# Optimization experiments

Measured on AMD Instinct MI355X. Metric: run time of the kernel, lower is better.

## Reference

```python
import jax, jax.numpy as jnp
import numpy as np

DIM = 1024
N_HEADS = 16
HEAD_DIM = DIM // N_HEADS
MLP_RATIO = 4
LN_EPS = 1e-5


def _layer_norm(x, w):
    xf = x.astype(jnp.float32)
    mu = jnp.mean(xf, axis=-1, keepdims=True)
    var = jnp.var(xf, axis=-1, keepdims=True)
    y = (xf - mu) / jnp.sqrt(var + LN_EPS)
    return y * w[None, None, :]


def _apply_rope(x, cos, sin):
    # x: (b, s, h, d); cos, sin: (s, d/2)
    c = jnp.concatenate([cos, cos], axis=-1)[None, :, None, :]  # (1,s,1,d)
    s_ = jnp.concatenate([sin, sin], axis=-1)[None, :, None, :]
    x1, x2 = jnp.split(x, 2, axis=-1)
    rot = jnp.concatenate([-x2, x1], axis=-1)
    return x * c + rot * s_


def setup_inputs() -> dict:
    key = jax.random.key(0)
    ks = jax.random.split(key, 12)
    b, s = 2, 2048
    x = jax.random.normal(ks[0], (b, s, DIM), dtype=jnp.float32)
    rot_cos = jax.random.uniform(ks[1], (1, s, 1, 1, HEAD_DIM), dtype=jnp.float32)
    rot_sin = jax.random.uniform(ks[2], (1, s, 1, 1, HEAD_DIM), dtype=jnp.float32)
    w_init = 0.02
    params = {
        'ln1_w': jnp.ones((DIM,), jnp.float32),
        'w_qkv': jax.random.normal(ks[3], (3 * DIM, DIM), jnp.float32) * w_init,
        'w_out': jax.random.normal(ks[4], (DIM, DIM), jnp.float32) * w_init,
        'ln2_w': jnp.ones((DIM,), jnp.float32),
        'w_mlp1': jax.random.normal(ks[5], (MLP_RATIO * DIM, DIM), jnp.float32) * w_init,
        'b_mlp1': jnp.zeros((MLP_RATIO * DIM,), jnp.float32),
        'w_mlp2': jax.random.normal(ks[6], (DIM, MLP_RATIO * DIM), jnp.float32) * w_init,
        'b_mlp2': jnp.zeros((DIM,), jnp.float32),
    }
    return {'x': x, 'rot_cos': rot_cos, 'rot_sin': rot_sin, **params}


def reference(x, rot_cos, rot_sin, ln1_w, w_qkv, w_out, ln2_w, w_mlp1, b_mlp1, w_mlp2, b_mlp2):
    b, s, _ = x.shape
    # _split_rotary: (1,s,1,1,hd) -> (s, hd/2)
    cos = rot_cos[0, :, 0, 0, : HEAD_DIM // 2]
    sin = rot_sin[0, :, 0, 0, : HEAD_DIM // 2]

    x_skip = x
    h1 = _layer_norm(x, ln1_w)
    qkv = jnp.einsum('bsd,ed->bse', h1, w_qkv).reshape(b, s, 3, N_HEADS, HEAD_DIM)
    q, k, v = qkv[:, :, 0], qkv[:, :, 1], qkv[:, :, 2]
    q = _apply_rope(q, cos, sin)
    k = _apply_rope(k, cos, sin)

    # causal SDPA, scale = 1/sqrt(head_dim) (flex_attention default)
    scale = 1.0 / np.sqrt(HEAD_DIM)
    scores = jnp.einsum('bqhd,bkhd->bhqk', q, k) * scale
    causal = jnp.tril(jnp.ones((s, s), dtype=bool))
    scores = jnp.where(causal[None, None], scores, -jnp.inf)
    attn = jax.nn.softmax(scores, axis=-1)
    o = jnp.einsum('bhqk,bkhd->bqhd', attn, v).reshape(b, s, DIM)

    # attn out + residual (eval: dropout off, scale=1)
    x = x_skip + jnp.einsum('bsd,ed->bse', o, w_out)

    # MLP with tanh GELU + residual
    h2 = _layer_norm(x, ln2_w)
    u = jnp.einsum('bsd,ed->bse', h2, w_mlp1) + b_mlp1
    u = jax.nn.gelu(u, approximate=True)
    m = jnp.einsum('bse,de->bsd', u, w_mlp2) + b_mlp2
    return x + m
```

## Files before the change

kernel.cpp:

```cpp
#include <hip/hip_runtime.h>
#include <hip/hip_bf16.h>
#include <math.h>


#define B_ 2
#define S_ 2048
#define D_ 1024
#define H_ 16
#define DH_ 64
#define MLP_ 4096
#define ROWS_ (B_ * S_)

typedef short bf16x8 __attribute__((ext_vector_type(8)));
typedef float f32x4 __attribute__((ext_vector_type(4)));
typedef unsigned short ushort_t;
typedef ushort_t u16x4 __attribute__((ext_vector_type(4)));
typedef unsigned int u32x2 __attribute__((ext_vector_type(2)));

__device__ __forceinline__ float wave_reduce_sum(float v) {
  #pragma unroll
  for (int off = 32; off > 0; off >>= 1) v += __shfl_down(v, off, 64);
  return v;
}

__device__ __forceinline__ ushort_t f2bf(float v) {
  __hip_bfloat16 h = __float2bfloat16(v);
  return *(ushort_t*)&h;
}
__device__ __forceinline__ float bf2f(ushort_t u) {
  unsigned int v = ((unsigned int)u) << 16;
  union { unsigned int i; float f; } c; c.i = v; return c.f;
}

__device__ __forceinline__ float exp2_fast(float x) {
#if __has_builtin(__builtin_amdgcn_exp2f)
  return __builtin_amdgcn_exp2f(x);
#else
  return exp2f(x);
#endif
}
__device__ __forceinline__ float rcp_fast(float x) {
#if __has_builtin(__builtin_amdgcn_rcpf)
  return __builtin_amdgcn_rcpf(x);
#else
  return 1.0f / x;
#endif
}

__device__ __forceinline__ void async_copy16(const void* g, void* l) {
  __builtin_amdgcn_global_load_lds(
      (const __attribute__((address_space(1))) void*)g,
      (__attribute__((address_space(3))) void*)l, 16, 0, 0);
}

__global__ __launch_bounds__(256) void cast_w_kernel(
    const float* __restrict__ s0, ushort_t* __restrict__ d0, int n0,
    const float* __restrict__ s1, ushort_t* __restrict__ d1, int n1,
    const float* __restrict__ s2, ushort_t* __restrict__ d2, int n2,
    const float* __restrict__ s3, ushort_t* __restrict__ d3, int n3) {
  const float* s; ushort_t* d; int n;
  switch (blockIdx.y) {
    case 0: s = s0; d = d0; n = n0; break;
    case 1: s = s1; d = d1; n = n1; break;
    case 2: s = s2; d = d2; n = n2; break;
    default: s = s3; d = d3; n = n3; break;
  }
  const int i = (blockIdx.x * 256 + threadIdx.x) * 4;
  if (i < n) {
    const float4 v = *reinterpret_cast<const float4*>(s + i);
    u16x4 o;
    o[0] = f2bf(v.x); o[1] = f2bf(v.y); o[2] = f2bf(v.z); o[3] = f2bf(v.w);
    *reinterpret_cast<u16x4*>(d + i) = o;
  }
}

__global__ __launch_bounds__(256) void ln_kernel(
    const float* __restrict__ x, const float* __restrict__ w,
    ushort_t* __restrict__ y) {
  const int row = blockIdx.x;
  const float4 v = reinterpret_cast<const float4*>(x + (size_t)row * D_)[threadIdx.x];
  float s  = v.x + v.y + v.z + v.w;
  float ss = v.x * v.x + v.y * v.y + v.z * v.z + v.w * v.w;
  __shared__ float red[8];
  const int wave = threadIdx.x >> 6, lane = threadIdx.x & 63;
  const float ws1 = wave_reduce_sum(s);
  const float ws2 = wave_reduce_sum(ss);
  if (lane == 0) { red[wave] = ws1; red[4 + wave] = ws2; }
  __syncthreads();
  const float tot  = red[0] + red[1] + red[2] + red[3];
  const float tot2 = red[4] + red[5] + red[6] + red[7];
  const float mu  = tot * (1.0f / D_);
  const float var = tot2 * (1.0f / D_) - mu * mu;
  const float inv = rsqrtf(var + 1e-5f);
  const float4 wv = reinterpret_cast<const float4*>(w)[threadIdx.x];
  u16x4 o;
  o[0] = f2bf((v.x - mu) * inv * wv.x);
  o[1] = f2bf((v.y - mu) * inv * wv.y);
  o[2] = f2bf((v.z - mu) * inv * wv.z);
  o[3] = f2bf((v.w - mu) * inv * wv.w);
  reinterpret_cast<u16x4*>(y + (size_t)row * D_)[threadIdx.x] = o;
}

__device__ __forceinline__ float gelu_tanh(float u) {
  const float p = u + 0.044715f * u * u * u;
  const float e = exp2_fast(-2.3022078f * p);
  return u * rcp_fast(1.0f + e);
}

template <int FUSE, int OUTBF, int QKV>
__global__ __launch_bounds__(256) void gemm_bt(
    const ushort_t* __restrict__ A, const ushort_t* __restrict__ W,
    const float* __restrict__ bias, const float* __restrict__ res,
    void* __restrict__ Cv, ushort_t* __restrict__ VtOut,
    int M, int N, int K, int sm, int sn, int rects_n) {
  __shared__ ushort_t As[3][128 * 32];
  __shared__ ushort_t Bs[3][128 * 32];
  const int tid = threadIdx.x;
  const int wave = tid >> 6, lane = tid & 63;
  const int l15 = lane & 15, quad = lane >> 4;

  const int lin = blockIdx.x;
  const int xcd = lin & 7, j = lin >> 3;
  const int rm = xcd / rects_n, rn = xcd % rects_n;
  const int m0 = (rm * sm + (j % sm)) * 128;
  const int n0 = (rn * sn + (j / sm)) * 128;
  const int wm = (wave & 1) * 64, wn = (wave >> 1) * 64;

  const int srow = tid >> 2;
  const int gcol = (((tid & 3) ^ ((srow >> 1) & 3)) * 8);
  const ushort_t* Ag = A + (size_t)(m0 + srow) * K + gcol;
  const ushort_t* Wg = W + (size_t)(n0 + srow) * K + gcol;

  f32x4 acc[4][4] = {};
  const int rslot = (quad ^ ((l15 >> 1) & 3)) * 8;

  const int NI = K >> 5;
  async_copy16(Ag,               &As[0][tid * 8]);
  async_copy16(Ag + 64 * K,      &As[0][2048 + tid * 8]);
  async_copy16(Wg,               &Bs[0][tid * 8]);
  async_copy16(Wg + 64 * K,      &Bs[0][2048 + tid * 8]);
  if (NI > 1) {
    async_copy16(Ag + 32,          &As[1][tid * 8]);
    async_copy16(Ag + 64 * K + 32, &As[1][2048 + tid * 8]);
    async_copy16(Wg + 32,          &Bs[1][tid * 8]);
    async_copy16(Wg + 64 * K + 32, &Bs[1][2048 + tid * 8]);
  }

  int st = 0;
  for (int i = 0; i < NI; ++i) {
    if (i + 1 < NI) asm volatile("s_waitcnt vmcnt(4)" ::: "memory");
    else            asm volatile("s_waitcnt vmcnt(0)" ::: "memory");
    __builtin_amdgcn_s_barrier();
    __builtin_amdgcn_sched_barrier(0);
    if (i + 2 < NI) {
      const int k2 = (i + 2) << 5;
      const int nb = (st >= 1) ? st - 1 : st + 2;
      async_copy16(Ag + k2,          &As[nb][tid * 8]);
      async_copy16(Ag + 64 * K + k2, &As[nb][2048 + tid * 8]);
      async_copy16(Wg + k2,          &Bs[nb][tid * 8]);
      async_copy16(Wg + 64 * K + k2, &Bs[nb][2048 + tid * 8]);
    }
    bf16x8 af[4], bfr[4];
    #pragma unroll
    for (int ii = 0; ii < 4; ++ii) {
      af[ii]  = *(const bf16x8*)&As[st][(wm + ii * 16 + l15) * 32 + rslot];
      bfr[ii] = *(const bf16x8*)&Bs[st][(wn + ii * 16 + l15) * 32 + rslot];
    }
    #pragma unroll
    for (int ii = 0; ii < 4; ++ii)
      #pragma unroll
      for (int jj = 0; jj < 4; ++jj)
        acc[ii][jj] = __builtin_amdgcn_mfma_f32_16x16x32_bf16(af[ii], bfr[jj], acc[ii][jj], 0, 0, 0);
    st = (st == 2) ? 0 : st + 1;
  }

  #pragma unroll
  for (int i = 0; i < 4; ++i) {
    const int mb = m0 + wm + i * 16 + quad * 4;
    #pragma unroll
    for (int jj = 0; jj < 4; ++jj) {
      const int n = n0 + wn + jj * 16 + l15;
      float cv[4];
      #pragma unroll
      for (int r = 0; r < 4; ++r) {
        float c = acc[i][jj][r];
        if (FUSE & 1) c += bias[n];
        if (FUSE & 2) c = gelu_tanh(c);
        if (FUSE & 4) c += res[(size_t)(mb + r) * N + n];
        cv[r] = c;
      }
      if (QKV && ((n0 + wn) >> 10) == 2) {
        const int d  = n & 63;
        const int hh = (n >> 6) & 15;
        const int bb = mb >> 11;
        const int ss = mb & (S_ - 1);
        u16x4 pk;
        #pragma unroll
        for (int r = 0; r < 4; ++r) pk[r] = f2bf(cv[r]);
        *(u16x4*)&VtOut[((size_t)(bb * H_ + hh) * DH_ + d) * S_ + ss] = pk;
      } else {
        #pragma unroll
        for (int r = 0; r < 4; ++r) {
          if (OUTBF) ((ushort_t*)Cv)[(size_t)(mb + r) * N + n] = f2bf(cv[r]);
          else       ((float*)Cv)[(size_t)(mb + r) * N + n]   = cv[r];
        }
      }
    }
  }
}

template <int FUSE, int OUTBF>
__global__ __launch_bounds__(256) void gemm64_bt(
    const ushort_t* __restrict__ A, const ushort_t* __restrict__ W,
    const float* __restrict__ bias, const float* __restrict__ res,
    void* __restrict__ Cv, int M, int N, int K, int sm, int sn, int rects_n) {
  __shared__ ushort_t As[2][64 * 64];
  __shared__ ushort_t Bs[2][128 * 64];
  const int tid = threadIdx.x;
  const int wave = tid >> 6, lane = tid & 63;
  const int l15 = lane & 15, quad = lane >> 4;

  const int lin = blockIdx.x;
  const int xcd = lin & 7, j = lin >> 3;
  const int rm = xcd / rects_n, rn = xcd % rects_n;
  const int m0 = (rm * sm + (j % sm)) * 64;
  const int n0 = (rn * sn + (j / sm)) * 128;
  const int wn = wave * 32;

  const int srow = tid >> 3;
  const int gcol = (((tid & 7) ^ (srow & 7)) * 8);
  const ushort_t* Ag = A + (size_t)(m0 + srow) * K + gcol;
  const ushort_t* Wg = W + (size_t)(n0 + srow) * K + gcol;

  f32x4 acc[4][2] = {};

  const int NI = K >> 6;
  #pragma unroll
  for (int i = 0; i < 2; ++i)
    async_copy16(Ag + (size_t)i * 32 * K, &As[0][i * 2048 + tid * 8]);
  #pragma unroll
  for (int i = 0; i < 4; ++i)
    async_copy16(Wg + (size_t)i * 32 * K, &Bs[0][i * 2048 + tid * 8]);

  for (int it = 0; it < NI; ++it) {
    const int st = it & 1;
    __syncthreads();
    if (it + 1 < NI) {
      const int k1 = (it + 1) << 6;
      #pragma unroll
      for (int i = 0; i < 2; ++i)
        async_copy16(Ag + (size_t)i * 32 * K + k1, &As[1 - st][i * 2048 + tid * 8]);
      #pragma unroll
      for (int i = 0; i < 4; ++i)
        async_copy16(Wg + (size_t)i * 32 * K + k1, &Bs[1 - st][i * 2048 + tid * 8]);
    }
    #pragma unroll
    for (int kk = 0; kk < 2; ++kk) {
      const int slot = (((kk * 4 + quad) ^ (l15 & 7)) * 8);
      bf16x8 af[4], bfr[2];
      #pragma unroll
      for (int i = 0; i < 4; ++i)
        af[i] = *(const bf16x8*)&As[st][(i * 16 + l15) * 64 + slot];
      #pragma unroll
      for (int jj = 0; jj < 2; ++jj)
        bfr[jj] = *(const bf16x8*)&Bs[st][(wn + jj * 16 + l15) * 64 + slot];
      #pragma unroll
      for (int i = 0; i < 4; ++i)
        #pragma unroll
        for (int jj = 0; jj < 2; ++jj)
          acc[i][jj] = __builtin_amdgcn_mfma_f32_16x16x32_bf16(af[i], bfr[jj], acc[i][jj], 0, 0, 0);
    }
  }

  #pragma unroll
  for (int i = 0; i < 4; ++i) {
    const int mb = m0 + i * 16 + quad * 4;
    #pragma unroll
    for (int jj = 0; jj < 2; ++jj) {
      const int n = n0 + wn + jj * 16 + l15;
      #pragma unroll
      for (int r = 0; r < 4; ++r) {
        float c = acc[i][jj][r];
        if (FUSE & 1) c += bias[n];
        if (FUSE & 2) c = gelu_tanh(c);
        if (FUSE & 4) c += res[(size_t)(mb + r) * N + n];
        if (OUTBF) ((ushort_t*)Cv)[(size_t)(mb + r) * N + n] = f2bf(c);
        else       ((float*)Cv)[(size_t)(mb + r) * N + n]   = c;
      }
    }
  }
}

__global__ __launch_bounds__(256) void rope_kernel(
    const ushort_t* __restrict__ qkv, const float* __restrict__ cosb,
    const float* __restrict__ sinb, ushort_t* __restrict__ Qo,
    ushort_t* __restrict__ Ko) {
  const int bs = blockIdx.x;
  const int s  = bs & (S_ - 1);
  const int b  = bs >> 11;
  const int t  = threadIdx.x;
  const ushort_t* base = qkv + (size_t)bs * (3 * D_);
  #pragma unroll
  for (int i = 0; i < 8; ++i) {
    const int e = i * 256 + t;
    const int which = e >> 10;
    const int rem = e & 1023;
    const int h = rem >> 6;
    const int d = rem & 63;
    const float val = bf2f(base[e]);
    float out;
    if (d < 32) {
      out = val * cosb[s * 64 + d] - bf2f(base[e + 32]) * sinb[s * 64 + d];
    } else {
      out = val * cosb[s * 64 + d - 32] + bf2f(base[e - 32]) * sinb[s * 64 + d - 32];
    }
    const size_t oidx = (((size_t)(b * H_ + h)) * S_ + s) * DH_ + d;
    if (which == 0) Qo[oidx] = f2bf(out * 0.18033688736f);
    else            Ko[oidx] = f2bf(out);
  }
}

#define PPAD 72

__global__ __launch_bounds__(256) void attn_kernel(
    const ushort_t* __restrict__ Qb, const ushort_t* __restrict__ Kb,
    const ushort_t* __restrict__ Vt, ushort_t* __restrict__ O) {
  __shared__ ushort_t Ks[2][64 * 64];
  __shared__ ushort_t Vs[2][64 * 64];
  __shared__ ushort_t Plds[4][2][16 * PPAD];

  const int tid  = threadIdx.x;
  const int wave = tid >> 6;
  const int lane = tid & 63;
  const int l15 = lane & 15, quad = lane >> 4;

  const int lin = blockIdx.x;
  const int bh  = lin & 31;
  const int g   = 15 - (lin >> 5);
  const int b = bh >> 4, h = bh & 15;
  const int q0 = g * 128 + wave * 32;

  const int nch_w   = (q0 >> 6) + 1;
  const int nch_max = 2 * g + 2;

  const ushort_t* Kbh = Kb + (size_t)bh * S_ * DH_;
  const ushort_t* Vbh = Vt + (size_t)bh * DH_ * S_;

  auto stage = [&](int buf, int c) {
    const int k0s = c << 6;
    #pragma unroll
    for (int i = 0; i < 2; ++i) {
      const int idx  = i * 256 + tid;
      const int row  = idx >> 3;
      const int slot = idx & 7;
      const int scol = ((slot ^ (row & 7)) * 8);
      async_copy16(Kbh + (size_t)(k0s + row) * DH_ + scol, &Ks[buf][idx * 8]);
      async_copy16(Vbh + (size_t)row * S_ + k0s + scol,    &Vs[buf][idx * 8]);
    }
  };

  bf16x8 qb[2][2];
  #pragma unroll
  for (int t = 0; t < 2; ++t) {
    const ushort_t* qptr = Qb + ((size_t)bh * S_ + q0 + t * 16 + l15) * DH_ + quad * 8;
    qb[t][0] = *(const bf16x8*)(qptr);
    qb[t][1] = *(const bf16x8*)(qptr + 32);
  }

  f32x4 o_acc[2][4] = {};
  float m_run[2] = {-1e30f, -1e30f}, l_run[2] = {0.0f, 0.0f};

  stage(0, 0);

  for (int c = 0; c < nch_max; ++c) {
    const int st = c & 1;
    __syncthreads();
    if (c + 1 < nch_max) stage(st ^ 1, c + 1);
    if (c >= nch_w) continue;
    const int k0 = c << 6;

    bf16x8 ka[4][2];
    #pragma unroll
    for (int kt = 0; kt < 4; ++kt) {
      const int row = kt * 16 + l15;
      const int bse = row * 64, rx = row & 7;
      ka[kt][0] = *(const bf16x8*)&Ks[st][bse + ((quad ^ rx) * 8)];
      ka[kt][1] = *(const bf16x8*)&Ks[st][bse + (((4 + quad) ^ rx) * 8)];
    }

    f32x4 s_t[2][4];
    __builtin_amdgcn_s_setprio(1);
    #pragma unroll
    for (int t = 0; t < 2; ++t)
      #pragma unroll
      for (int kt = 0; kt < 4; ++kt) {
        f32x4 z = {0.0f, 0.0f, 0.0f, 0.0f};
        z = __builtin_amdgcn_mfma_f32_16x16x32_bf16(ka[kt][0], qb[t][0], z, 0, 0, 0);
        z = __builtin_amdgcn_mfma_f32_16x16x32_bf16(ka[kt][1], qb[t][1], z, 0, 0, 0);
        s_t[t][kt] = z;
      }
    __builtin_amdgcn_s_setprio(0);

    if (c == nch_w - 1) {
      #pragma unroll
      for (int t = 0; t < 2; ++t) {
        const int query = q0 + t * 16 + l15;
        #pragma unroll
        for (int kt = 0; kt < 4; ++kt)
          #pragma unroll
          for (int r = 0; r < 4; ++r)
            if (k0 + kt * 16 + quad * 4 + r > query) s_t[t][kt][r] = -1e30f;
      }
    }

    #pragma unroll
    for (int t = 0; t < 2; ++t) {
      float mx = -1e30f;
      #pragma unroll
      for (int kt = 0; kt < 4; ++kt)
        #pragma unroll
        for (int r = 0; r < 4; ++r) mx = fmaxf(mx, s_t[t][kt][r]);
      mx = fmaxf(mx, __shfl_xor(mx, 16, 64));
      mx = fmaxf(mx, __shfl_xor(mx, 32, 64));
      const float m_new = fmaxf(m_run[t], mx);
      const float alpha = exp2_fast(m_run[t] - m_new);
      float rs = 0.0f;
      #pragma unroll
      for (int kt = 0; kt < 4; ++kt)
        #pragma unroll
        for (int r = 0; r < 4; ++r) {
          const float e = exp2_fast(s_t[t][kt][r] - m_new);
          s_t[t][kt][r] = e;
          rs += e;
        }
      rs += __shfl_xor(rs, 16, 64);
      rs += __shfl_xor(rs, 32, 64);
      l_run[t] = l_run[t] * alpha + rs;
      m_run[t] = m_new;
      #pragma unroll
      for (int mt = 0; mt < 4; ++mt)
        #pragma unroll
        for (int r = 0; r < 4; ++r) o_acc[t][mt][r] *= alpha;
    }

    bf16x8 va[4][2];
    #pragma unroll
    for (int mt = 0; mt < 4; ++mt) {
      const int row = mt * 16 + l15;
      const int bse = row * 64, rx = row & 7;
      va[mt][0] = *(const bf16x8*)&Vs[st][bse + ((quad ^ rx) * 8)];
      va[mt][1] = *(const bf16x8*)&Vs[st][bse + (((4 + quad) ^ rx) * 8)];
    }

    #pragma unroll
    for (int t = 0; t < 2; ++t) {
      ushort_t* Pw = &Plds[wave][t][0];
      #pragma unroll
      for (int kt = 0; kt < 4; ++kt) {
        u32x2 wpair;
        wpair[0] = (unsigned)f2bf(s_t[t][kt][0]) | ((unsigned)f2bf(s_t[t][kt][1]) << 16);
        wpair[1] = (unsigned)f2bf(s_t[t][kt][2]) | ((unsigned)f2bf(s_t[t][kt][3]) << 16);
        *(u32x2*)&Pw[l15 * PPAD + kt * 16 + quad * 4] = wpair;
      }
      asm volatile("s_waitcnt lgkmcnt(0)" ::: "memory");
      const bf16x8 pb0 = *(const bf16x8*)&Pw[l15 * PPAD + quad * 8];
      const bf16x8 pb1 = *(const bf16x8*)&Pw[l15 * PPAD + 32 + quad * 8];
      __builtin_amdgcn_s_setprio(1);
      #pragma unroll
      for (int mt = 0; mt < 4; ++mt) {
        o_acc[t][mt] = __builtin_amdgcn_mfma_f32_16x16x32_bf16(va[mt][0], pb0, o_acc[t][mt], 0, 0, 0);
        o_acc[t][mt] = __builtin_amdgcn_mfma_f32_16x16x32_bf16(va[mt][1], pb1, o_acc[t][mt], 0, 0, 0);
      }
      __builtin_amdgcn_s_setprio(0);
    }
  }

  #pragma unroll
  for (int t = 0; t < 2; ++t) {
    const float inv = 1.0f / l_run[t];
    #pragma unroll
    for (int mt = 0; mt < 4; ++mt) {
      u16x4 pk;
      #pragma unroll
      for (int r = 0; r < 4; ++r) pk[r] = f2bf(o_acc[t][mt][r] * inv);
      *(u16x4*)&O[(((size_t)b * S_ + q0 + t * 16 + l15) * H_ + h) * DH_ + mt * 16 + quad * 4] = pk;
    }
  }
}

extern "C" void kernel_launch(void* const* d_in, const int* in_sizes, int n_in,
                              void* d_out, int out_size, void* d_ws, size_t ws_size,
                              hipStream_t stream) {
  const float* x       = (const float*)d_in[0];
  const float* rot_cos = (const float*)d_in[1];
  const float* rot_sin = (const float*)d_in[2];
  const float* ln1_w   = (const float*)d_in[3];
  const float* w_qkv   = (const float*)d_in[4];
  const float* w_out   = (const float*)d_in[5];
  const float* ln2_w   = (const float*)d_in[6];
  const float* w_mlp1  = (const float*)d_in[7];
  const float* b_mlp1  = (const float*)d_in[8];
  const float* w_mlp2  = (const float*)d_in[9];
  const float* b_mlp2  = (const float*)d_in[10];
  float* out = (float*)d_out;

  char* wsb = (char*)d_ws;
  const size_t MB = 1u << 20;
  ushort_t* h1_bf  = (ushort_t*)(wsb + 0 * MB);
  ushort_t* qkv_bf = (ushort_t*)(wsb + 8 * MB);
  ushort_t* q_bf   = (ushort_t*)(wsb + 32 * MB);
  ushort_t* k_bf   = (ushort_t*)(wsb + 40 * MB);
  ushort_t* v_t    = (ushort_t*)(wsb + 48 * MB);
  ushort_t* o_bf   = (ushort_t*)(wsb + 56 * MB);
  float*    x2     = (float*)   (wsb + 64 * MB);
  ushort_t* u_bf   = (ushort_t*)(wsb + 80 * MB);
  ushort_t* wq_bf  = (ushort_t*)(wsb + 112 * MB);
  ushort_t* wo_bf  = (ushort_t*)(wsb + 118 * MB);
  ushort_t* w1_bf  = (ushort_t*)(wsb + 120 * MB);
  ushort_t* w2_bf  = (ushort_t*)(wsb + 128 * MB);
  (void)ws_size; (void)in_sizes; (void)n_in; (void)out_size;

  dim3 b256(256);

  cast_w_kernel<<<dim3(4096, 4), b256, 0, stream>>>(
      w_qkv, wq_bf, 3 * D_ * D_, w_out, wo_bf, D_ * D_,
      w_mlp1, w1_bf, MLP_ * D_, w_mlp2, w2_bf, MLP_ * D_);
  ln_kernel<<<dim3(ROWS_), b256, 0, stream>>>(x, ln1_w, h1_bf);
  gemm_bt<0, 1, 1><<<dim3(768), b256, 0, stream>>>(
      h1_bf, wq_bf, nullptr, nullptr, qkv_bf, v_t, ROWS_, 3 * D_, D_, 16, 6, 4);
  rope_kernel<<<dim3(ROWS_), b256, 0, stream>>>(qkv_bf, rot_cos, rot_sin, q_bf, k_bf);
  attn_kernel<<<dim3(512), b256, 0, stream>>>(q_bf, k_bf, v_t, o_bf);
  gemm64_bt<4, 0><<<dim3(512), b256, 0, stream>>>(
      o_bf, wo_bf, nullptr, x, x2, ROWS_, D_, D_, 16, 4, 2);
  ln_kernel<<<dim3(ROWS_), b256, 0, stream>>>(x2, ln2_w, h1_bf);
  gemm_bt<3, 1, 0><<<dim3(1024), b256, 0, stream>>>(
      h1_bf, w1_bf, b_mlp1, nullptr, u_bf, nullptr, ROWS_, MLP_, D_, 16, 8, 4);
  gemm64_bt<5, 0><<<dim3(512), b256, 0, stream>>>(
      u_bf, w2_bf, b_mlp2, x2, out, ROWS_, D_, MLP_, 16, 4, 2);
}
```

Baseline: 364.4 us.

## Triple-buffer GEMM loads, reorder attention blocks, and skip lazy softmax rescales

The 64x128 GEMM moves from a double-buffered to a triple-buffered cp.async pipeline, prefetching two K-tiles ahead and replacing __syncthreads with a vmcnt wait plus s_barrier, so global-load latency is hidden better. The attention kernel changes its query-block launch order so the first half of blocks run heavy tiles in descending order and the rest ascending, to balance causal work. The online softmax skips the rescale of O and l whenever the new max exceeds the running max by at most 8 in log2 space, trading some exp headroom for less rescale work. Shared memory per GEMM block grows by half, which may lower occupancy.

After: 366.8 us. About the same (+0.7%).

```diff
diff --git a/kernel.cpp b/kernel.cpp
--- a/kernel.cpp
+++ b/kernel.cpp
@@ -214,8 +214,8 @@
     const ushort_t* __restrict__ A, const ushort_t* __restrict__ W,
     const float* __restrict__ bias, const float* __restrict__ res,
     void* __restrict__ Cv, int M, int N, int K, int sm, int sn, int rects_n) {
-  __shared__ ushort_t As[2][64 * 64];
-  __shared__ ushort_t Bs[2][128 * 64];
+  __shared__ ushort_t As[3][64 * 64];
+  __shared__ ushort_t Bs[3][128 * 64];
   const int tid = threadIdx.x;
   const int wave = tid >> 6, lane = tid & 63;
   const int l15 = lane & 15, quad = lane >> 4;
@@ -241,18 +241,30 @@
   #pragma unroll
   for (int i = 0; i < 4; ++i)
     async_copy16(Wg + (size_t)i * 32 * K, &Bs[0][i * 2048 + tid * 8]);
-
+  if (NI > 1) {
+    #pragma unroll
+    for (int i = 0; i < 2; ++i)
+      async_copy16(Ag + (size_t)i * 32 * K + 64, &As[1][i * 2048 + tid * 8]);
+    #pragma unroll
+    for (int i = 0; i < 4; ++i)
+      async_copy16(Wg + (size_t)i * 32 * K + 64, &Bs[1][i * 2048 + tid * 8]);
+  }
+
+  int st = 0;
   for (int it = 0; it < NI; ++it) {
-    const int st = it & 1;
-    __syncthreads();
-    if (it + 1 < NI) {
-      const int k1 = (it + 1) << 6;
+    if (it + 1 < NI) asm volatile("s_waitcnt vmcnt(6)" ::: "memory");
+    else             asm volatile("s_waitcnt vmcnt(0)" ::: "memory");
+    __builtin_amdgcn_s_barrier();
+    __builtin_amdgcn_sched_barrier(0);
+    if (it + 2 < NI) {
+      const int k2 = (it + 2) << 6;
+      const int nb = (st >= 1) ? st - 1 : st + 2;
       #pragma unroll
       for (int i = 0; i < 2; ++i)
-        async_copy16(Ag + (size_t)i * 32 * K + k1, &As[1 - st][i * 2048 + tid * 8]);
+        async_copy16(Ag + (size_t)i * 32 * K + k2, &As[nb][i * 2048 + tid * 8]);
       #pragma unroll
       for (int i = 0; i < 4; ++i)
-        async_copy16(Wg + (size_t)i * 32 * K + k1, &Bs[1 - st][i * 2048 + tid * 8]);
+        async_copy16(Wg + (size_t)i * 32 * K + k2, &Bs[nb][i * 2048 + tid * 8]);
     }
     #pragma unroll
     for (int kk = 0; kk < 2; ++kk) {
@@ -270,6 +282,7 @@
         for (int jj = 0; jj < 2; ++jj)
           acc[i][jj] = __builtin_amdgcn_mfma_f32_16x16x32_bf16(af[i], bfr[jj], acc[i][jj], 0, 0, 0);
     }
+    st = (st == 2) ? 0 : st + 1;
   }
 
   #pragma unroll
@@ -336,7 +349,8 @@
 
   const int lin = blockIdx.x;
   const int bh  = lin & 31;
-  const int g   = 15 - (lin >> 5);
+  const int u   = lin >> 5;
+  const int g   = (u < 8) ? (15 - u) : (u - 8);
   const int b = bh >> 4, h = bh & 15;
   const int q0 = g * 128 + wave * 32;
 
@@ -422,25 +436,28 @@
         for (int r = 0; r < 4; ++r) mx = fmaxf(mx, s_t[t][kt][r]);
       mx = fmaxf(mx, __shfl_xor(mx, 16, 64));
       mx = fmaxf(mx, __shfl_xor(mx, 32, 64));
-      const float m_new = fmaxf(m_run[t], mx);
-      const float alpha = exp2_fast(m_run[t] - m_new);
+      if (!__all(mx <= m_run[t] + 8.0f)) {
+        const float m_new = fmaxf(m_run[t], mx);
+        const float alpha = exp2_fast(m_run[t] - m_new);
+        l_run[t] *= alpha;
+        #pragma unroll
+        for (int mt = 0; mt < 4; ++mt)
+          #pragma unroll
+          for (int r = 0; r < 4; ++r) o_acc[t][mt][r] *= alpha;
+        m_run[t] = m_new;
+      }
       float rs = 0.0f;
       #pragma unroll
       for (int kt = 0; kt < 4; ++kt)
         #pragma unroll
         for (int r = 0; r < 4; ++r) {
-          const float e = exp2_fast(s_t[t][kt][r] - m_new);
+          const float e = exp2_fast(s_t[t][kt][r] - m_run[t]);
           s_t[t][kt][r] = e;
           rs += e;
         }
       rs += __shfl_xor(rs, 16, 64);
       rs += __shfl_xor(rs, 32, 64);
-      l_run[t] = l_run[t] * alpha + rs;
-      m_run[t] = m_new;
-      #pragma unroll
-      for (int mt = 0; mt < 4; ++mt)
-        #pragma unroll
-        for (int r = 0; r < 4; ++r) o_acc[t][mt][r] *= alpha;
+      l_run[t] += rs;
     }
 
     bf16x8 va[4][2];
```
